# Kernel tuning notes

Measured on AMD Instinct MI355X. Metric: run time of the kernel, lower is better.

## Reference

```python
import jax, jax.numpy as jnp
import numpy as np


def _wkv(time_decay, time_first, k, v):
    # time_decay, time_first: [C]; k, v: [B, T, C]
    w = -jnp.exp(time_decay)  # per-channel decay (negative)
    u = time_first
    B, T, C = k.shape
    aa = jnp.zeros((B, C), dtype=k.dtype)
    bb = jnp.zeros((B, C), dtype=k.dtype)
    pp = jnp.full((B, C), -1e38, dtype=k.dtype)  # running max exponent

    def step(carry, kv_t):
        aa, bb, pp = carry
        kt, vt = kv_t  # [B, C] each
        # output with bonus u for current token
        ww = u + kt
        q = jnp.maximum(pp, ww)
        e1 = jnp.exp(pp - q)
        e2 = jnp.exp(ww - q)
        y_t = (e1 * aa + e2 * vt) / (e1 * bb + e2)
        # decayed state update
        ww2 = pp + w
        q2 = jnp.maximum(ww2, kt)
        e1b = jnp.exp(ww2 - q2)
        e2b = jnp.exp(kt - q2)
        new_carry = (e1b * aa + e2b * vt, e1b * bb + e2b, q2)
        return new_carry, y_t

    ks = jnp.transpose(k, (1, 0, 2))  # [T, B, C]
    vs = jnp.transpose(v, (1, 0, 2))
    _, ys = jax.lax.scan(step, (aa, bb, pp), (ks, vs))
    return jnp.transpose(ys, (1, 0, 2))  # [B, T, C]


def setup_inputs() -> dict:
    key = jax.random.key(0)
    k1, k2, k3, k4 = jax.random.split(key, 4)
    B, T, C = 8, 1024, 2048
    return {
        "batch_size": B,
        "seq_len": T,
        "embedding_dim": C,
        "time_decay": jax.random.normal(k1, (C,), dtype=jnp.float32),
        "time_first": jax.random.normal(k2, (C,), dtype=jnp.float32),
        "k": jax.random.normal(k3, (B, T, C), dtype=jnp.float32),
        "v": jax.random.normal(k4, (B, T, C), dtype=jnp.float32),
    }


def reference(batch_size, seq_len, embedding_dim, time_decay, time_first, k, v):
    assert seq_len <= 1024  # T_max
    return _wkv(time_decay, time_first, k, v)
```

## Files before the change

### kernel.cpp

```cpp
#include <hip/hip_runtime.h>


#define T_FIX 1024
#define NCH   16
#define CHL   (T_FIX / NCH)

__global__ __launch_bounds__(256)
void wkv_pass1(const float* __restrict__ td,
               const float* __restrict__ k,
               const float* __restrict__ v,
               float* __restrict__ aa_s,
               float* __restrict__ bb_s,
               float* __restrict__ pp_s,
               int B, int C)
{
    int gid = blockIdx.x * blockDim.x + threadIdx.x;
    if (gid >= B * C * NCH) return;
    int c   = gid % C;
    int rem = gid / C;
    int j   = rem % NCH;
    int b   = rem / NCH;

    float w = -__expf(td[c]);

    const size_t base = ((size_t)b * T_FIX + (size_t)j * CHL) * C + c;
    const float* kp = k + base;
    const float* vp = v + base;

    float aa = 0.f, bb = 0.f, pp = -1e38f;
    #pragma unroll 8
    for (int t = 0; t < CHL; ++t) {
        float kt = kp[(size_t)t * C];
        float vt = vp[(size_t)t * C];
        float ww2 = pp + w;
        float q2  = fmaxf(ww2, kt);
        float e1b = __expf(ww2 - q2);
        float e2b = __expf(kt - q2);
        aa = e1b * aa + e2b * vt;
        bb = e1b * bb + e2b;
        pp = q2;
    }
    size_t sidx = (size_t)j * B * C + (size_t)b * C + c;
    aa_s[sidx] = aa;
    bb_s[sidx] = bb;
    pp_s[sidx] = pp;
}

__global__ __launch_bounds__(256)
void wkv_pass2(const float* __restrict__ td,
               float* __restrict__ aa_s,
               float* __restrict__ bb_s,
               float* __restrict__ pp_s,
               int B, int C)
{
    int gid = blockIdx.x * blockDim.x + threadIdx.x;
    if (gid >= B * C) return;
    int c = gid % C;

    float w  = -__expf(td[c]);
    float Lw = (float)CHL * w;

    float aa = 0.f, bb = 0.f, pp = -1e38f;
    const size_t BC = (size_t)B * C;
    #pragma unroll
    for (int j = 0; j < NCH; ++j) {
        size_t idx = (size_t)j * BC + gid;
        float ca = aa_s[idx];
        float cb = bb_s[idx];
        float cm = pp_s[idx];
        aa_s[idx] = aa;
        bb_s[idx] = bb;
        pp_s[idx] = pp;
        float ppd = pp + Lw;
        float pn  = fmaxf(ppd, cm);
        float ea  = __expf(ppd - pn);
        float eb  = __expf(cm - pn);
        aa = ea * aa + eb * ca;
        bb = ea * bb + eb * cb;
        pp = pn;
    }
}

__global__ __launch_bounds__(256)
void wkv_pass3(const float* __restrict__ td,
               const float* __restrict__ tf,
               const float* __restrict__ k,
               const float* __restrict__ v,
               const float* __restrict__ aa_s,
               const float* __restrict__ bb_s,
               const float* __restrict__ pp_s,
               float* __restrict__ y,
               int B, int C)
{
    int gid = blockIdx.x * blockDim.x + threadIdx.x;
    if (gid >= B * C * NCH) return;
    int c   = gid % C;
    int rem = gid / C;
    int j   = rem % NCH;
    int b   = rem / NCH;

    float w = -__expf(td[c]);
    float u = tf[c];

    const size_t base = ((size_t)b * T_FIX + (size_t)j * CHL) * C + c;
    const float* kp = k + base;
    const float* vp = v + base;
    float*       yp = y + base;

    size_t sidx = (size_t)j * B * C + (size_t)b * C + c;
    float aa = aa_s[sidx];
    float bb = bb_s[sidx];
    float pp = pp_s[sidx];

    #pragma unroll 8
    for (int t = 0; t < CHL; ++t) {
        float kt = kp[(size_t)t * C];
        float vt = vp[(size_t)t * C];
        float ww = u + kt;
        float q  = fmaxf(pp, ww);
        float e1 = __expf(pp - q);
        float e2 = __expf(ww - q);
        yp[(size_t)t * C] = __fdividef(e1 * aa + e2 * vt, e1 * bb + e2);
        float ww2 = pp + w;
        float q2  = fmaxf(ww2, kt);
        float e1b = __expf(ww2 - q2);
        float e2b = __expf(kt - q2);
        aa = e1b * aa + e2b * vt;
        bb = e1b * bb + e2b;
        pp = q2;
    }
}

extern "C" void kernel_launch(void* const* d_in, const int* in_sizes, int n_in,
                              void* d_out, int out_size, void* d_ws, size_t ws_size,
                              hipStream_t stream)
{
    const float* td = (const float*)d_in[3];
    const float* tf = (const float*)d_in[4];
    const float* k  = (const float*)d_in[5];
    const float* v  = (const float*)d_in[6];
    float*       y  = (float*)d_out;

    const int C   = in_sizes[3];
    const int BTC = in_sizes[5];
    const int B   = BTC / (T_FIX * C);

    const size_t N = (size_t)B * C * NCH;
    float* aa_s = (float*)d_ws;
    float* bb_s = aa_s + N;
    float* pp_s = bb_s + N;

    const int block = 256;
    const int grid13 = (int)((N + block - 1) / block);
    const int grid2  = (B * C + block - 1) / block;

    wkv_pass1<<<grid13, block, 0, stream>>>(td, k, v, aa_s, bb_s, pp_s, B, C);
    wkv_pass2<<<grid2,  block, 0, stream>>>(td, aa_s, bb_s, pp_s, B, C);
    wkv_pass3<<<grid13, block, 0, stream>>>(td, tf, k, v, aa_s, bb_s, pp_s, y, B, C);
}
```

Before: 216.8 us.

## Vectorize WKV chunked scan with float4, fold carry pass into emit kernel

Doubles the chunk count and has each thread handle four channels through float4 loads and stores of k, v, y and the chunk states. It also removes the separate sequential carry kernel: each emit thread recombines the preceding chunk summaries itself, and k/v loads are batched eight timesteps ahead for more memory-level parallelism. This cuts a launch and narrow scalar loads, but adds redundant prefix work per thread (up to 31 chunk combines) and leaves a quarter as many threads per chunk.

```diff
diff --git a/kernel.cpp b/kernel.cpp
--- a/kernel.cpp
+++ b/kernel.cpp
@@ -2,132 +2,152 @@
 
 
 #define T_FIX 1024
-#define NCH   16
+#define NCH   32
 #define CHL   (T_FIX / NCH)
+#define BATCH 8
+
+__device__ __forceinline__ void wkv_step(float& aa, float& bb, float& pp,
+                                         float w, float kt, float vt)
+{
+    float ww2 = pp + w;
+    float q2  = fmaxf(ww2, kt);
+    float e1  = __expf(ww2 - q2);
+    float e2  = __expf(kt - q2);
+    aa = fmaf(e1, aa, e2 * vt);
+    bb = fmaf(e1, bb, e2);
+    pp = q2;
+}
+
+#define F4TOA(a, f) { a[0] = (f).x; a[1] = (f).y; a[2] = (f).z; a[3] = (f).w; }
 
 __global__ __launch_bounds__(256)
-void wkv_pass1(const float* __restrict__ td,
-               const float* __restrict__ k,
-               const float* __restrict__ v,
-               float* __restrict__ aa_s,
-               float* __restrict__ bb_s,
-               float* __restrict__ pp_s,
-               int B, int C)
+void wkv_states(const float* __restrict__ td,
+                const float* __restrict__ k,
+                const float* __restrict__ v,
+                float* __restrict__ aa_s,
+                float* __restrict__ bb_s,
+                float* __restrict__ pp_s,
+                int B, int C)
 {
+    const int C4  = C >> 2;
     int gid = blockIdx.x * blockDim.x + threadIdx.x;
-    if (gid >= B * C * NCH) return;
-    int c   = gid % C;
-    int rem = gid / C;
+    if (gid >= B * NCH * C4) return;
+    int c4  = gid % C4;
+    int rem = gid / C4;
     int j   = rem % NCH;
     int b   = rem / NCH;
+    int c   = c4 << 2;
 
-    float w = -__expf(td[c]);
+    float4 tdv = *(const float4*)(td + c);
+    float w[4] = { -__expf(tdv.x), -__expf(tdv.y), -__expf(tdv.z), -__expf(tdv.w) };
 
     const size_t base = ((size_t)b * T_FIX + (size_t)j * CHL) * C + c;
     const float* kp = k + base;
     const float* vp = v + base;
 
-    float aa = 0.f, bb = 0.f, pp = -1e38f;
-    #pragma unroll 8
-    for (int t = 0; t < CHL; ++t) {
-        float kt = kp[(size_t)t * C];
-        float vt = vp[(size_t)t * C];
-        float ww2 = pp + w;
-        float q2  = fmaxf(ww2, kt);
-        float e1b = __expf(ww2 - q2);
-        float e2b = __expf(kt - q2);
-        aa = e1b * aa + e2b * vt;
-        bb = e1b * bb + e2b;
-        pp = q2;
+    float aa[4] = {0.f, 0.f, 0.f, 0.f};
+    float bb[4] = {0.f, 0.f, 0.f, 0.f};
+    float pp[4] = {-1e38f, -1e38f, -1e38f, -1e38f};
+
+    for (int tb = 0; tb < CHL; tb += BATCH) {
+        float4 kb[BATCH], vb[BATCH];
+        #pragma unroll
+        for (int i = 0; i < BATCH; ++i) {
+            kb[i] = *(const float4*)(kp + (size_t)(tb + i) * C);
+            vb[i] = *(const float4*)(vp + (size_t)(tb + i) * C);
+        }
+        #pragma unroll
+        for (int i = 0; i < BATCH; ++i) {
+            float ka[4], va[4];
+            F4TOA(ka, kb[i]); F4TOA(va, vb[i]);
+            #pragma unroll
+            for (int cc = 0; cc < 4; ++cc)
+                wkv_step(aa[cc], bb[cc], pp[cc], w[cc], ka[cc], va[cc]);
+        }
     }
-    size_t sidx = (size_t)j * B * C + (size_t)b * C + c;
-    aa_s[sidx] = aa;
-    bb_s[sidx] = bb;
-    pp_s[sidx] = pp;
+
+    size_t sidx = ((size_t)j * B + b) * C + c;
+    *(float4*)(aa_s + sidx) = make_float4(aa[0], aa[1], aa[2], aa[3]);
+    *(float4*)(bb_s + sidx) = make_float4(bb[0], bb[1], bb[2], bb[3]);
+    *(float4*)(pp_s + sidx) = make_float4(pp[0], pp[1], pp[2], pp[3]);
 }
 
 __global__ __launch_bounds__(256)
-void wkv_pass2(const float* __restrict__ td,
-               float* __restrict__ aa_s,
-               float* __restrict__ bb_s,
-               float* __restrict__ pp_s,
-               int B, int C)
+void wkv_emit(const float* __restrict__ td,
+              const float* __restrict__ tf,
+              const float* __restrict__ k,
+              const float* __restrict__ v,
+              const float* __restrict__ aa_s,
+              const float* __restrict__ bb_s,
+              const float* __restrict__ pp_s,
+              float* __restrict__ y,
+              int B, int C)
 {
+    const int C4  = C >> 2;
     int gid = blockIdx.x * blockDim.x + threadIdx.x;
-    if (gid >= B * C) return;
-    int c = gid % C;
-
-    float w  = -__expf(td[c]);
-    float Lw = (float)CHL * w;
-
-    float aa = 0.f, bb = 0.f, pp = -1e38f;
-    const size_t BC = (size_t)B * C;
-    #pragma unroll
-    for (int j = 0; j < NCH; ++j) {
-        size_t idx = (size_t)j * BC + gid;
-        float ca = aa_s[idx];
-        float cb = bb_s[idx];
-        float cm = pp_s[idx];
-        aa_s[idx] = aa;
-        bb_s[idx] = bb;
-        pp_s[idx] = pp;
-        float ppd = pp + Lw;
-        float pn  = fmaxf(ppd, cm);
-        float ea  = __expf(ppd - pn);
-        float eb  = __expf(cm - pn);
-        aa = ea * aa + eb * ca;
-        bb = ea * bb + eb * cb;
-        pp = pn;
-    }
-}
-
-__global__ __launch_bounds__(256)
-void wkv_pass3(const float* __restrict__ td,
-               const float* __restrict__ tf,
-               const float* __restrict__ k,
-               const float* __restrict__ v,
-               const float* __restrict__ aa_s,
-               const float* __restrict__ bb_s,
-               const float* __restrict__ pp_s,
-               float* __restrict__ y,
-               int B, int C)
-{
-    int gid = blockIdx.x * blockDim.x + threadIdx.x;
-    if (gid >= B * C * NCH) return;
-    int c   = gid % C;
-    int rem = gid / C;
+    if (gid >= B * NCH * C4) return;
+    int c4  = gid % C4;
+    int rem = gid / C4;
     int j   = rem % NCH;
     int b   = rem / NCH;
+    int c   = c4 << 2;
 
-    float w = -__expf(td[c]);
-    float u = tf[c];
+    float4 tdv = *(const float4*)(td + c);
+    float4 tfv = *(const float4*)(tf + c);
+    float w[4] = { -__expf(tdv.x), -__expf(tdv.y), -__expf(tdv.z), -__expf(tdv.w) };
+    float u[4];  F4TOA(u, tfv);
+
+    float aa[4] = {0.f, 0.f, 0.f, 0.f};
+    float bb[4] = {0.f, 0.f, 0.f, 0.f};
+    float pp[4] = {-1e38f, -1e38f, -1e38f, -1e38f};
+
+    for (int jj = 0; jj < j; ++jj) {
+        size_t sidx = ((size_t)jj * B + b) * C + c;
+        float4 c_a = *(const float4*)(aa_s + sidx);
+        float4 c_b = *(const float4*)(bb_s + sidx);
+        float4 c_m = *(const float4*)(pp_s + sidx);
+        float ca[4], cb[4], cm[4];
+        F4TOA(ca, c_a); F4TOA(cb, c_b); F4TOA(cm, c_m);
+        #pragma unroll
+        for (int cc = 0; cc < 4; ++cc) {
+            float ppd = pp[cc] + (float)CHL * w[cc];
+            float pn  = fmaxf(ppd, cm[cc]);
+            float ea  = __expf(ppd - pn);
+            float eb  = __expf(cm[cc] - pn);
+            aa[cc] = fmaf(ea, aa[cc], eb * ca[cc]);
+            bb[cc] = fmaf(ea, bb[cc], eb * cb[cc]);
+            pp[cc] = pn;
+        }
+    }
 
     const size_t base = ((size_t)b * T_FIX + (size_t)j * CHL) * C + c;
     const float* kp = k + base;
     const float* vp = v + base;
     float*       yp = y + base;
 
-    size_t sidx = (size_t)j * B * C + (size_t)b * C + c;
-    float aa = aa_s[sidx];
-    float bb = bb_s[sidx];
-    float pp = pp_s[sidx];
-
-    #pragma unroll 8
-    for (int t = 0; t < CHL; ++t) {
-        float kt = kp[(size_t)t * C];
-        float vt = vp[(size_t)t * C];
-        float ww = u + kt;
-        float q  = fmaxf(pp, ww);
-        float e1 = __expf(pp - q);
-        float e2 = __expf(ww - q);
-        yp[(size_t)t * C] = __fdividef(e1 * aa + e2 * vt, e1 * bb + e2);
-        float ww2 = pp + w;
-        float q2  = fmaxf(ww2, kt);
-        float e1b = __expf(ww2 - q2);
-        float e2b = __expf(kt - q2);
-        aa = e1b * aa + e2b * vt;
-        bb = e1b * bb + e2b;
-        pp = q2;
+    for (int tb = 0; tb < CHL; tb += BATCH) {
+        float4 kb[BATCH], vb[BATCH];
+        #pragma unroll
+        for (int i = 0; i < BATCH; ++i) {
+            kb[i] = *(const float4*)(kp + (size_t)(tb + i) * C);
+            vb[i] = *(const float4*)(vp + (size_t)(tb + i) * C);
+        }
+        #pragma unroll
+        for (int i = 0; i < BATCH; ++i) {
+            float ka[4], va[4], ya[4];
+            F4TOA(ka, kb[i]); F4TOA(va, vb[i]);
+            #pragma unroll
+            for (int cc = 0; cc < 4; ++cc) {
+                float ww = u[cc] + ka[cc];
+                float q  = fmaxf(pp[cc], ww);
+                float e1 = __expf(pp[cc] - q);
+                float e2 = __expf(ww - q);
+                ya[cc] = __fdividef(fmaf(e1, aa[cc], e2 * va[cc]),
+                                    fmaf(e1, bb[cc], e2));
+                wkv_step(aa[cc], bb[cc], pp[cc], w[cc], ka[cc], va[cc]);
+            }
+            *(float4*)(yp + (size_t)(tb + i) * C) = make_float4(ya[0], ya[1], ya[2], ya[3]);
+        }
     }
 }
 
@@ -150,11 +170,10 @@
     float* bb_s = aa_s + N;
     float* pp_s = bb_s + N;
 
-    const int block = 256;
-    const int grid13 = (int)((N + block - 1) / block);
-    const int grid2  = (B * C + block - 1) / block;
+    const int block   = 256;
+    const int threads = B * NCH * (C >> 2);
+    const int grid    = (threads + block - 1) / block;
 
-    wkv_pass1<<<grid13, block, 0, stream>>>(td, k, v, aa_s, bb_s, pp_s, B, C);
-    wkv_pass2<<<grid2,  block, 0, stream>>>(td, aa_s, bb_s, pp_s, B, C);
-    wkv_pass3<<<grid13, block, 0, stream>>>(td, tf, k, v, aa_s, bb_s, pp_s, y, B, C);
+    wkv_states<<<grid, block, 0, stream>>>(td, k, v, aa_s, bb_s, pp_s, B, C);
+    wkv_emit  <<<grid, block, 0, stream>>>(td, tf, k, v, aa_s, bb_s, pp_s, y, B, C);
 }
```

After: 216.6 us. About the same (-0.1%).
